# Optimization experiments

Measured on AMD Instinct MI355X. Metric: run time of the kernel, lower is better.

Reference implementation:

```python
import jax, jax.numpy as jnp
import numpy as np

KERNEL_SIZES = (3, 5, 7)
NUM_HEAD = 6
DIM = 192
K_SCALES = 3
HEADS_PER_SCALE = NUM_HEAD // K_SCALES  # 2
HEAD_DIM = DIM // NUM_HEAD              # 32
SCALE = HEAD_DIM ** -0.5


def _nbr_idx(L, K):
    # NATTEN non-causal, dilation=1: window centered on query, clamped at edges.
    start = jnp.clip(jnp.arange(L) - K // 2, 0, L - K)
    return start[:, None] + jnp.arange(K)  # [L, K]


def _na3d_branch(xi, K):
    # xi: [B, D, H, W, C] with C = 3 * HEADS_PER_SCALE * HEAD_DIM
    B, D, H, W, C = xi.shape
    qkv = xi.reshape(B, D, H, W, 3, HEADS_PER_SCALE, HEAD_DIM).transpose(4, 0, 5, 1, 2, 3, 6)
    q, k, v = qkv[0] * SCALE, qkv[1], qkv[2]  # each [B, h, D, H, W, hd]

    idd, idh, idw = _nbr_idx(D, K), _nbr_idx(H, K), _nbr_idx(W, K)

    def gather(t):
        t = jnp.take(t, idd, axis=2)  # [B,h,D,K,H,W,hd]
        t = jnp.take(t, idh, axis=4)  # [B,h,D,K,H,K,W,hd]
        t = jnp.take(t, idw, axis=6)  # [B,h,D,K,H,K,W,K,hd]
        return t

    kn = gather(k)
    vn = gather(v)
    # attention logits over the K^3 neighborhood per query
    attn = jnp.einsum('bndhwc,bndihjwkc->bndhwijk', q, kn)
    attn = jax.nn.softmax(attn.reshape(B, HEADS_PER_SCALE, D, H, W, K ** 3), axis=-1)
    attn = attn.reshape(B, HEADS_PER_SCALE, D, H, W, K, K, K)
    y = jnp.einsum('bndhwijk,bndihjwkc->bndhwc', attn, vn)
    # [B,h,D,H,W,hd] -> [B,D,H,W,h*hd]
    return y.transpose(0, 2, 3, 4, 1, 5).reshape(B, D, H, W, HEADS_PER_SCALE * HEAD_DIM)


def setup_inputs() -> dict:
    key = jax.random.key(0)
    k0, k1, k2 = jax.random.split(key, 3)
    x = jax.random.normal(k0, (1, 8, 24, 24, DIM), dtype=jnp.float32)
    W_qkv = jax.random.normal(k1, (DIM, 3 * DIM), dtype=jnp.float32) * 0.02
    b_qkv = jnp.zeros((3 * DIM,), dtype=jnp.float32)
    W_proj = jax.random.normal(k2, (DIM, DIM), dtype=jnp.float32) * 0.02
    b_proj = jnp.zeros((DIM,), dtype=jnp.float32)
    return {'x': x, 'W_qkv': W_qkv, 'b_qkv': b_qkv, 'W_proj': W_proj, 'b_proj': b_proj}


def reference(x, W_qkv, b_qkv, W_proj, b_proj):
    qkv = x @ W_qkv + b_qkv  # [B,D,H,W,3*DIM]
    # torch.split with channels [DIM, DIM, DIM]
    chunks = jnp.split(qkv, K_SCALES, axis=4)
    ys = [_na3d_branch(chunks[i], KERNEL_SIZES[i]) for i in range(K_SCALES)]
    y = jnp.concatenate(ys, axis=4)  # [B,D,H,W,DIM]
    return y @ W_proj + b_proj
```

## Files before the change

kernel.cpp:

```cpp
#include <hip/hip_runtime.h>

typedef unsigned short ushort_t;
typedef unsigned int uint_t;
typedef __attribute__((ext_vector_type(8))) short short8;
typedef __attribute__((ext_vector_type(4))) float f32x4;

constexpr int DD = 8, HH = 24, WW = 24;
constexpr int NQ = DD * HH * WW;
constexpr int CIN = 192;
constexpr int CQKV = 576;
constexpr int KP = 576;
constexpr float ATT_SCALE = 0.17677669529663687f;
constexpr int NROW = DD * HH;

__device__ __forceinline__ ushort_t bf16h(float x) {
    uint_t u = __float_as_uint(x);
    u += 0x7FFFu + ((u >> 16) & 1u);
    return (ushort_t)(u >> 16);
}
__device__ __forceinline__ float bf16f(ushort_t h) {
    return __uint_as_float(((uint_t)h) << 16);
}
__device__ __forceinline__ void unpack8(uint4 u, float* f) {
    f[0] = __uint_as_float(u.x << 16); f[1] = __uint_as_float(u.x & 0xffff0000u);
    f[2] = __uint_as_float(u.y << 16); f[3] = __uint_as_float(u.y & 0xffff0000u);
    f[4] = __uint_as_float(u.z << 16); f[5] = __uint_as_float(u.z & 0xffff0000u);
    f[6] = __uint_as_float(u.w << 16); f[7] = __uint_as_float(u.w & 0xffff0000u);
}

__global__ __launch_bounds__(256)
void convert_w_kernel(const float* __restrict__ Wq, const float* __restrict__ Wp,
                      ushort_t* __restrict__ Bq, ushort_t* __restrict__ Bp)
{
    __shared__ float T[32][36];
    int b = blockIdx.x;
    const float* W; ushort_t* Bb; int N;
    int kt, nt;
    if (b < 108) { W = Wq; Bb = Bq; N = CQKV; kt = b % 6; nt = b / 6; }
    else         { b -= 108; W = Wp; Bb = Bp; N = CIN; kt = b % 6; nt = b / 6; }
    const int k0 = kt * 32, n0 = nt * 32;
    const int tid = threadIdx.x;

    #pragma unroll
    for (int p = 0; p < 4; ++p) {
        int e = p * 256 + tid;
        int r = e >> 5, c = e & 31;
        T[c][r] = W[(long)(k0 + r) * N + n0 + c];
    }
    __syncthreads();
    const int n = tid >> 3;
    const int k4 = (tid & 7) * 4;
    float4 v = *(const float4*)(&T[n][k4]);
    ushort4 hv, lv;
    hv.x = bf16h(v.x); lv.x = bf16h(v.x - bf16f(hv.x));
    hv.y = bf16h(v.y); lv.y = bf16h(v.y - bf16f(hv.y));
    hv.z = bf16h(v.z); lv.z = bf16h(v.z - bf16f(hv.z));
    hv.w = bf16h(v.w); lv.w = bf16h(v.w - bf16f(hv.w));
    ushort_t* row = Bb + (long)(n0 + n) * KP + k0 + k4;
    *(ushort4*)(row)           = hv;
    *(ushort4*)(row + CIN)     = hv;
    *(ushort4*)(row + 2 * CIN) = lv;
}

template<bool BF16OUT>
__global__ __launch_bounds__(256)
void gemm_mfma_kernel(const float* __restrict__ A, const ushort_t* __restrict__ Bb,
                      const float* __restrict__ bias, void* __restrict__ Cout, int N)
{
    __shared__ ushort_t As[64][72];
    __shared__ ushort_t Bs[64][72];
    __shared__ float Ct[64][68];

    const int tid = threadIdx.x;
    const int bm = blockIdx.x * 64;
    const int bn = blockIdx.y * 64;

    const int wv = tid >> 6;
    const int lane = tid & 63;
    const int lm = lane & 15;
    const int quad = lane >> 4;
    const int wr = (wv >> 1) * 32;
    const int wc = (wv & 1) * 32;

    const int ar = tid >> 4;
    const int ac4 = (tid & 15) * 4;
    const int br0 = tid >> 3;
    const int bc0 = (tid & 7) * 8;

    f32x4 acc[2][2] = {};

    for (int kk = 0; kk < KP; kk += 64) {
        const int p3 = kk / 192;
        const int k0 = kk - p3 * 192;
        float4 av[4];
        #pragma unroll
        for (int p = 0; p < 4; ++p)
            av[p] = *(const float4*)(A + (long)(bm + ar + p * 16) * CIN + k0 + ac4);
        uint4 b0 = *(const uint4*)(Bb + (long)(bn + br0) * KP + kk + bc0);
        uint4 b1 = *(const uint4*)(Bb + (long)(bn + br0 + 32) * KP + kk + bc0);
        __syncthreads();
        #pragma unroll
        for (int p = 0; p < 4; ++p) {
            float4 v = av[p];
            ushort4 hv;
            hv.x = bf16h(v.x); hv.y = bf16h(v.y); hv.z = bf16h(v.z); hv.w = bf16h(v.w);
            if (p3 == 1) {
                hv.x = bf16h(v.x - bf16f(hv.x));
                hv.y = bf16h(v.y - bf16f(hv.y));
                hv.z = bf16h(v.z - bf16f(hv.z));
                hv.w = bf16h(v.w - bf16f(hv.w));
            }
            *(ushort4*)(&As[ar + p * 16][ac4]) = hv;
        }
        *(uint4*)(&Bs[br0][bc0]) = b0;
        *(uint4*)(&Bs[br0 + 32][bc0]) = b1;
        __syncthreads();

        #pragma unroll
        for (int ks = 0; ks < 64; ks += 32) {
            short8 af0 = *(const short8*)(&As[wr + lm][ks + quad * 8]);
            short8 af1 = *(const short8*)(&As[wr + 16 + lm][ks + quad * 8]);
            short8 bf0 = *(const short8*)(&Bs[wc + lm][ks + quad * 8]);
            short8 bf1 = *(const short8*)(&Bs[wc + 16 + lm][ks + quad * 8]);
            acc[0][0] = __builtin_amdgcn_mfma_f32_16x16x32_bf16(af0, bf0, acc[0][0], 0, 0, 0);
            acc[0][1] = __builtin_amdgcn_mfma_f32_16x16x32_bf16(af0, bf1, acc[0][1], 0, 0, 0);
            acc[1][0] = __builtin_amdgcn_mfma_f32_16x16x32_bf16(af1, bf0, acc[1][0], 0, 0, 0);
            acc[1][1] = __builtin_amdgcn_mfma_f32_16x16x32_bf16(af1, bf1, acc[1][1], 0, 0, 0);
        }
    }

    #pragma unroll
    for (int tc = 0; tc < 2; ++tc) {
        const float bv = bias[bn + wc + tc * 16 + lm];
        #pragma unroll
        for (int tr = 0; tr < 2; ++tr) {
            #pragma unroll
            for (int reg = 0; reg < 4; ++reg)
                Ct[wr + tr * 16 + quad * 4 + reg][wc + tc * 16 + lm] = acc[tr][tc][reg] + bv;
        }
    }
    __syncthreads();
    const int orow = tid >> 4;
    const int oc4 = (tid & 15) * 4;
    #pragma unroll
    for (int p = 0; p < 4; ++p) {
        const int r = orow + p * 16;
        float4 v = *(const float4*)(&Ct[r][oc4]);
        if (BF16OUT) {
            ushort4 hv;
            hv.x = bf16h(v.x); hv.y = bf16h(v.y); hv.z = bf16h(v.z); hv.w = bf16h(v.w);
            *(ushort4*)((ushort_t*)Cout + (long)(bm + r) * N + bn + oc4) = hv;
        } else {
            *(float4*)((float*)Cout + (long)(bm + r) * N + bn + oc4) = v;
        }
    }
}

constexpr int KROW = 72;
constexpr int RBUF = WW * KROW;

constexpr int EB0 = 0;
constexpr int EB1 = NROW * 2 * WW * 2;
constexpr int EB2 = EB1 + NROW * 3 * WW * 2;
constexpr int ETOT = EB2 + NROW * 4 * WW * 2;

template<int K>
__device__ __forceinline__
void split_chunk(const ushort_t* __restrict__ qkv,
                 float* __restrict__ accs, float* __restrict__ stats,
                 int r, int c, int nchunks, int scale, int ebase,
                 int w, int hd, int d8, int tid,
                 ushort_t* __restrict__ ksh, ushort_t* __restrict__ vsh)
{
    const int i0 = 2 * c;
    const int ni = (K - i0) < 2 ? (K - i0) : 2;
    const int NT = ni * K;

    const int dq = r / HH, hq = r % HH;
    int sd = dq - K / 2; sd = sd < 0 ? 0 : (sd > DD - K ? DD - K : sd);
    int sh = hq - K / 2; sh = sh < 0 ? 0 : (sh > HH - K ? HH - K : sh);
    int sw = w  - K / 2; sw = sw < 0 ? 0 : (sw > WW - K ? WW - K : sw);

    const int q = (dq * HH + hq) * WW + w;

    uint4 qu = *(const uint4*)(qkv + (long)q * CQKV + scale * 192 + hd * 32 + d8 * 8);
    float qf[8];
    unpack8(qu, qf);
    #pragma unroll
    for (int t = 0; t < 8; ++t) qf[t] *= ATT_SCALE;

    const int lw = tid >> 3;
    const int c8 = (tid & 7) * 8;

    auto load_kv = [&](int buf, int t) {
        int i = i0 + t / K;
        int j = t - (t / K) * K;
        const ushort_t* p = qkv + (long)(((sd + i) * HH + (sh + j)) * WW + lw) * CQKV
                          + scale * 192 + c8;
        uint4 kk = *(const uint4*)(p + 64);
        uint4 vv = *(const uint4*)(p + 128);
        *(uint4*)(ksh + buf * RBUF + lw * KROW + c8) = kk;
        *(uint4*)(vsh + buf * RBUF + lw * KROW + c8) = vv;
    };

    float m = -1e30f, sum = 0.f;
    float acc[8] = {};
    const int choff = hd * 32 + d8 * 8;

    load_kv(0, 0);
    if (NT > 1) load_kv(1, 1);

    for (int t = 0; t < NT; ++t) {
        __syncthreads();
        if (t + 2 < NT) load_kv((t + 2) % 3, t + 2);

        const ushort_t* kb = ksh + (t % 3) * RBUF + choff;
        float lg[K];
        #pragma unroll
        for (int n = 0; n < K; ++n) {
            uint4 ku = *(const uint4*)(kb + (sw + n) * KROW);
            float kf[8];
            unpack8(ku, kf);
            float p = qf[0] * kf[0] + qf[1] * kf[1] + qf[2] * kf[2] + qf[3] * kf[3]
                    + qf[4] * kf[4] + qf[5] * kf[5] + qf[6] * kf[6] + qf[7] * kf[7];
            p += __shfl_xor(p, 1);
            p += __shfl_xor(p, 2);
            lg[n] = p;
        }
        float mloc = lg[0];
        #pragma unroll
        for (int n = 1; n < K; ++n) mloc = fmaxf(mloc, lg[n]);
        float mnew = fmaxf(m, mloc);
        float alpha = __expf(m - mnew);
        m = mnew;
        sum *= alpha;
        #pragma unroll
        for (int d = 0; d < 8; ++d) acc[d] *= alpha;

        const ushort_t* vb = vsh + (t % 3) * RBUF + choff;
        #pragma unroll
        for (int n = 0; n < K; ++n) {
            float pr = __expf(lg[n] - mnew);
            sum += pr;
            uint4 vu = *(const uint4*)(vb + (sw + n) * KROW);
            float vf[8];
            unpack8(vu, vf);
            #pragma unroll
            for (int d = 0; d < 8; ++d) acc[d] += pr * vf[d];
        }
    }

    const int e = ebase + ((r * nchunks + c) * WW + w) * 2 + hd;
    if (d8 == 0) {
        stats[2 * e]     = m;
        stats[2 * e + 1] = sum;
    }
    float* ap = accs + (long)e * 32 + d8 * 8;
    *(float4*)(ap)     = make_float4(acc[0], acc[1], acc[2], acc[3]);
    *(float4*)(ap + 4) = make_float4(acc[4], acc[5], acc[6], acc[7]);
}

__global__ __launch_bounds__(192)
void na3d_split_kernel(const ushort_t* __restrict__ qkv,
                       float* __restrict__ accs, float* __restrict__ stats)
{
    __shared__ alignas(16) ushort_t ksh[3 * RBUF];
    __shared__ alignas(16) ushort_t vsh[3 * RBUF];

    const int tid = threadIdx.x;
    const int w  = tid >> 3;
    const int hd = (tid >> 2) & 1;
    const int d8 = tid & 3;

    const int bid = blockIdx.x;
    if (bid < NROW * 4) {
        int r = bid >> 2, c = bid & 3;
        split_chunk<7>(qkv, accs, stats, r, c, 4, 2, EB2, w, hd, d8, tid, ksh, vsh);
    } else if (bid < NROW * 4 + NROW * 3) {
        int t = bid - NROW * 4;
        int r = t / 3, c = t - (t / 3) * 3;
        split_chunk<5>(qkv, accs, stats, r, c, 3, 1, EB1, w, hd, d8, tid, ksh, vsh);
    } else {
        int t = bid - NROW * 7;
        int r = t >> 1, c = t & 1;
        split_chunk<3>(qkv, accs, stats, r, c, 2, 0, EB0, w, hd, d8, tid, ksh, vsh);
    }
}

__global__ __launch_bounds__(256)
void na3d_combine_kernel(const float* __restrict__ accs,
                         const float* __restrict__ stats,
                         float* __restrict__ y)
{
    const int n = blockIdx.x * 256 + threadIdx.x;
    constexpr int PER_SCALE = NROW * WW * 2 * 8;
    const int scale = n / PER_SCALE;
    const int rem = n - scale * PER_SCALE;
    const int d4 = rem & 7;
    const int hd = (rem >> 3) & 1;
    const int t  = rem >> 4;
    const int w  = t % WW;
    const int row = t / WW;

    const int CK = scale == 0 ? 2 : (scale == 1 ? 3 : 4);
    const int ebase = scale == 0 ? EB0 : (scale == 1 ? EB1 : EB2);

    float mv[4], sv[4];
    float M = -1e30f;
    for (int c = 0; c < CK; ++c) {
        int e = ebase + ((row * CK + c) * WW + w) * 2 + hd;
        mv[c] = stats[2 * e];
        sv[c] = stats[2 * e + 1];
        M = fmaxf(M, mv[c]);
    }
    float S = 0.f;
    float4 o = make_float4(0.f, 0.f, 0.f, 0.f);
    for (int c = 0; c < CK; ++c) {
        int e = ebase + ((row * CK + c) * WW + w) * 2 + hd;
        float wgt = __expf(mv[c] - M);
        S += sv[c] * wgt;
        float4 a = *(const float4*)(accs + (long)e * 32 + d4 * 4);
        o.x += wgt * a.x; o.y += wgt * a.y; o.z += wgt * a.z; o.w += wgt * a.w;
    }
    const float rs = 1.0f / S;
    o.x *= rs; o.y *= rs; o.z *= rs; o.w *= rs;

    const int q = row * WW + w;
    *(float4*)(y + (long)q * CIN + scale * 64 + hd * 32 + d4 * 4) = o;
}

extern "C" void kernel_launch(void* const* d_in, const int* in_sizes, int n_in,
                              void* d_out, int out_size, void* d_ws, size_t ws_size,
                              hipStream_t stream)
{
    const float* x      = (const float*)d_in[0];
    const float* W_qkv  = (const float*)d_in[1];
    const float* b_qkv  = (const float*)d_in[2];
    const float* W_proj = (const float*)d_in[3];
    const float* b_proj = (const float*)d_in[4];
    float* out = (float*)d_out;

    float* accs    = (float*)d_ws;
    float* stats   = accs + (long)ETOT * 32;
    float* y       = stats + 2 * ETOT;
    ushort_t* qkvb = (ushort_t*)(y + (long)NQ * CIN);
    ushort_t* Wbq  = qkvb + (long)NQ * CQKV;
    ushort_t* Wbp  = Wbq + (long)CQKV * KP;

    convert_w_kernel<<<dim3(144), 256, 0, stream>>>(W_qkv, W_proj, Wbq, Wbp);

    gemm_mfma_kernel<true><<<dim3(NQ / 64, CQKV / 64), 256, 0, stream>>>(x, Wbq, b_qkv, qkvb, CQKV);

    na3d_split_kernel<<<dim3(NROW * (4 + 3 + 2)), 192, 0, stream>>>(qkvb, accs, stats);
    na3d_combine_kernel<<<dim3(3 * NQ * 16 / 256), 256, 0, stream>>>(accs, stats, y);

    gemm_mfma_kernel<false><<<dim3(NQ / 64, CIN / 64), 256, 0, stream>>>(y, Wbp, b_proj, out, CIN);
}
```

Before: 122.7 us.

## Fuse split-softmax combine into output projection GEMM via shared-memory bf16 split

Merges the combine kernel (which merges partial softmax chunks into y) into the projection GEMM. Each block recomputes its 64 query rows of y across all 192 channels, splits them into bf16 hi/lo parts in shared memory, and runs MFMA against the converted W_proj. This drops one kernel launch and the fp32 y round trip through global memory. In exchange, each of the 3 column-blocks per row tile redoes the combine work, and the larger shared-memory footprint may lower occupancy.

```diff
diff --git a/kernel.cpp b/kernel.cpp
--- a/kernel.cpp
+++ b/kernel.cpp
@@ -27,6 +27,11 @@
     f[4] = __uint_as_float(u.z << 16); f[5] = __uint_as_float(u.z & 0xffff0000u);
     f[6] = __uint_as_float(u.w << 16); f[7] = __uint_as_float(u.w & 0xffff0000u);
 }
+
+constexpr int EB0 = 0;
+constexpr int EB1 = NROW * 2 * WW * 2;
+constexpr int EB2 = EB1 + NROW * 3 * WW * 2;
+constexpr int ETOT = EB2 + NROW * 4 * WW * 2;
 
 __global__ __launch_bounds__(256)
 void convert_w_kernel(const float* __restrict__ Wq, const float* __restrict__ Wp,
@@ -62,10 +67,9 @@
     *(ushort4*)(row + 2 * CIN) = lv;
 }
 
-template<bool BF16OUT>
 __global__ __launch_bounds__(256)
-void gemm_mfma_kernel(const float* __restrict__ A, const ushort_t* __restrict__ Bb,
-                      const float* __restrict__ bias, void* __restrict__ Cout, int N)
+void gemm1_kernel(const float* __restrict__ A, const ushort_t* __restrict__ Bb,
+                  const float* __restrict__ bias, ushort_t* __restrict__ Cout)
 {
     __shared__ ushort_t As[64][72];
     __shared__ ushort_t Bs[64][72];
@@ -74,6 +78,7 @@
     const int tid = threadIdx.x;
     const int bm = blockIdx.x * 64;
     const int bn = blockIdx.y * 64;
+    const int N = CQKV;
 
     const int wv = tid >> 6;
     const int lane = tid & 63;
@@ -146,23 +151,14 @@
     for (int p = 0; p < 4; ++p) {
         const int r = orow + p * 16;
         float4 v = *(const float4*)(&Ct[r][oc4]);
-        if (BF16OUT) {
-            ushort4 hv;
-            hv.x = bf16h(v.x); hv.y = bf16h(v.y); hv.z = bf16h(v.z); hv.w = bf16h(v.w);
-            *(ushort4*)((ushort_t*)Cout + (long)(bm + r) * N + bn + oc4) = hv;
-        } else {
-            *(float4*)((float*)Cout + (long)(bm + r) * N + bn + oc4) = v;
-        }
+        ushort4 hv;
+        hv.x = bf16h(v.x); hv.y = bf16h(v.y); hv.z = bf16h(v.z); hv.w = bf16h(v.w);
+        *(ushort4*)(Cout + (long)(bm + r) * N + bn + oc4) = hv;
     }
 }
 
 constexpr int KROW = 72;
 constexpr int RBUF = WW * KROW;
-
-constexpr int EB0 = 0;
-constexpr int EB1 = NROW * 2 * WW * 2;
-constexpr int EB2 = EB1 + NROW * 3 * WW * 2;
-constexpr int ETOT = EB2 + NROW * 4 * WW * 2;
 
 template<int K>
 __device__ __forceinline__
@@ -287,46 +283,125 @@
     }
 }
 
+constexpr int YST = 200;
+
 __global__ __launch_bounds__(256)
-void na3d_combine_kernel(const float* __restrict__ accs,
-                         const float* __restrict__ stats,
-                         float* __restrict__ y)
-{
-    const int n = blockIdx.x * 256 + threadIdx.x;
-    constexpr int PER_SCALE = NROW * WW * 2 * 8;
-    const int scale = n / PER_SCALE;
-    const int rem = n - scale * PER_SCALE;
-    const int d4 = rem & 7;
-    const int hd = (rem >> 3) & 1;
-    const int t  = rem >> 4;
-    const int w  = t % WW;
-    const int row = t / WW;
-
-    const int CK = scale == 0 ? 2 : (scale == 1 ? 3 : 4);
-    const int ebase = scale == 0 ? EB0 : (scale == 1 ? EB1 : EB2);
-
-    float mv[4], sv[4];
-    float M = -1e30f;
-    for (int c = 0; c < CK; ++c) {
-        int e = ebase + ((row * CK + c) * WW + w) * 2 + hd;
-        mv[c] = stats[2 * e];
-        sv[c] = stats[2 * e + 1];
-        M = fmaxf(M, mv[c]);
-    }
-    float S = 0.f;
-    float4 o = make_float4(0.f, 0.f, 0.f, 0.f);
-    for (int c = 0; c < CK; ++c) {
-        int e = ebase + ((row * CK + c) * WW + w) * 2 + hd;
-        float wgt = __expf(mv[c] - M);
-        S += sv[c] * wgt;
-        float4 a = *(const float4*)(accs + (long)e * 32 + d4 * 4);
-        o.x += wgt * a.x; o.y += wgt * a.y; o.z += wgt * a.z; o.w += wgt * a.w;
-    }
-    const float rs = 1.0f / S;
-    o.x *= rs; o.y *= rs; o.z *= rs; o.w *= rs;
-
-    const int q = row * WW + w;
-    *(float4*)(y + (long)q * CIN + scale * 64 + hd * 32 + d4 * 4) = o;
+void combine_gemm2_kernel(const float* __restrict__ accs, const float* __restrict__ stats,
+                          const ushort_t* __restrict__ Bb, const float* __restrict__ bias,
+                          float* __restrict__ out)
+{
+    __shared__ union {
+        struct { ushort_t yhi[64][YST]; ushort_t ylo[64][YST]; ushort_t Bs[64][72]; } s;
+        float Ct[64][68];
+    } u;
+
+    const int tid = threadIdx.x;
+    const int bm = blockIdx.x * 64;
+    const int bn = blockIdx.y * 64;
+
+    {
+        const int ql = tid >> 2;
+        const int q = bm + ql;
+        const int row = q / WW;
+        const int w = q - row * WW;
+        const int chb = (tid & 3) * 48;
+        #pragma unroll
+        for (int c4 = 0; c4 < 12; ++c4) {
+            const int ch = chb + c4 * 4;
+            const int scale = ch >> 6;
+            const int rem = ch & 63;
+            const int hd = rem >> 5;
+            const int d4 = (rem >> 2) & 7;
+            const int CK = scale == 0 ? 2 : (scale == 1 ? 3 : 4);
+            const int ebase = scale == 0 ? EB0 : (scale == 1 ? EB1 : EB2);
+
+            float mv[4], sv[4];
+            float M = -1e30f;
+            for (int c = 0; c < CK; ++c) {
+                int e = ebase + ((row * CK + c) * WW + w) * 2 + hd;
+                mv[c] = stats[2 * e];
+                sv[c] = stats[2 * e + 1];
+                M = fmaxf(M, mv[c]);
+            }
+            float S = 0.f;
+            float4 o = make_float4(0.f, 0.f, 0.f, 0.f);
+            for (int c = 0; c < CK; ++c) {
+                int e = ebase + ((row * CK + c) * WW + w) * 2 + hd;
+                float wgt = __expf(mv[c] - M);
+                S += sv[c] * wgt;
+                float4 a = *(const float4*)(accs + (long)e * 32 + d4 * 4);
+                o.x += wgt * a.x; o.y += wgt * a.y; o.z += wgt * a.z; o.w += wgt * a.w;
+            }
+            const float rs = 1.0f / S;
+            o.x *= rs; o.y *= rs; o.z *= rs; o.w *= rs;
+
+            ushort4 hv, lv;
+            hv.x = bf16h(o.x); lv.x = bf16h(o.x - bf16f(hv.x));
+            hv.y = bf16h(o.y); lv.y = bf16h(o.y - bf16f(hv.y));
+            hv.z = bf16h(o.z); lv.z = bf16h(o.z - bf16f(hv.z));
+            hv.w = bf16h(o.w); lv.w = bf16h(o.w - bf16f(hv.w));
+            *(ushort4*)(&u.s.yhi[ql][ch]) = hv;
+            *(ushort4*)(&u.s.ylo[ql][ch]) = lv;
+        }
+    }
+    __syncthreads();
+
+    const int wv = tid >> 6;
+    const int lane = tid & 63;
+    const int lm = lane & 15;
+    const int quad = lane >> 4;
+    const int wr = (wv >> 1) * 32;
+    const int wc = (wv & 1) * 32;
+
+    const int br0 = tid >> 3;
+    const int bc0 = (tid & 7) * 8;
+
+    f32x4 acc[2][2] = {};
+
+    for (int kk = 0; kk < KP; kk += 64) {
+        const int p3 = kk / 192;
+        const int k0 = kk - p3 * 192;
+        uint4 b0 = *(const uint4*)(Bb + (long)(bn + br0) * KP + kk + bc0);
+        uint4 b1 = *(const uint4*)(Bb + (long)(bn + br0 + 32) * KP + kk + bc0);
+        __syncthreads();
+        *(uint4*)(&u.s.Bs[br0][bc0]) = b0;
+        *(uint4*)(&u.s.Bs[br0 + 32][bc0]) = b1;
+        __syncthreads();
+
+        const ushort_t* ybase = (p3 == 1) ? &u.s.ylo[0][0] : &u.s.yhi[0][0];
+        #pragma unroll
+        for (int ks = 0; ks < 64; ks += 32) {
+            short8 af0 = *(const short8*)(ybase + (wr + lm) * YST + k0 + ks + quad * 8);
+            short8 af1 = *(const short8*)(ybase + (wr + 16 + lm) * YST + k0 + ks + quad * 8);
+            short8 bf0 = *(const short8*)(&u.s.Bs[wc + lm][ks + quad * 8]);
+            short8 bf1 = *(const short8*)(&u.s.Bs[wc + 16 + lm][ks + quad * 8]);
+            acc[0][0] = __builtin_amdgcn_mfma_f32_16x16x32_bf16(af0, bf0, acc[0][0], 0, 0, 0);
+            acc[0][1] = __builtin_amdgcn_mfma_f32_16x16x32_bf16(af0, bf1, acc[0][1], 0, 0, 0);
+            acc[1][0] = __builtin_amdgcn_mfma_f32_16x16x32_bf16(af1, bf0, acc[1][0], 0, 0, 0);
+            acc[1][1] = __builtin_amdgcn_mfma_f32_16x16x32_bf16(af1, bf1, acc[1][1], 0, 0, 0);
+        }
+    }
+
+    __syncthreads();
+    #pragma unroll
+    for (int tc = 0; tc < 2; ++tc) {
+        const float bv = bias[bn + wc + tc * 16 + lm];
+        #pragma unroll
+        for (int tr = 0; tr < 2; ++tr) {
+            #pragma unroll
+            for (int reg = 0; reg < 4; ++reg)
+                u.Ct[wr + tr * 16 + quad * 4 + reg][wc + tc * 16 + lm] = acc[tr][tc][reg] + bv;
+        }
+    }
+    __syncthreads();
+    const int orow = tid >> 4;
+    const int oc4 = (tid & 15) * 4;
+    #pragma unroll
+    for (int p = 0; p < 4; ++p) {
+        const int r = orow + p * 16;
+        float4 v = *(const float4*)(&u.Ct[r][oc4]);
+        *(float4*)(out + (long)(bm + r) * CIN + bn + oc4) = v;
+    }
 }
 
 extern "C" void kernel_launch(void* const* d_in, const int* in_sizes, int n_in,
@@ -342,17 +417,15 @@
 
     float* accs    = (float*)d_ws;
     float* stats   = accs + (long)ETOT * 32;
-    float* y       = stats + 2 * ETOT;
-    ushort_t* qkvb = (ushort_t*)(y + (long)NQ * CIN);
+    ushort_t* qkvb = (ushort_t*)(stats + 2 * ETOT);
     ushort_t* Wbq  = qkvb + (long)NQ * CQKV;
     ushort_t* Wbp  = Wbq + (long)CQKV * KP;
 
     convert_w_kernel<<<dim3(144), 256, 0, stream>>>(W_qkv, W_proj, Wbq, Wbp);
 
-    gemm_mfma_kernel<true><<<dim3(NQ / 64, CQKV / 64), 256, 0, stream>>>(x, Wbq, b_qkv, qkvb, CQKV);
+    gemm1_kernel<<<dim3(NQ / 64, CQKV / 64), 256, 0, stream>>>(x, Wbq, b_qkv, qkvb);
 
     na3d_split_kernel<<<dim3(NROW * (4 + 3 + 2)), 192, 0, stream>>>(qkvb, accs, stats);
-    na3d_combine_kernel<<<dim3(3 * NQ * 16 / 256), 256, 0, stream>>>(accs, stats, y);
-
-    gemm_mfma_kernel<false><<<dim3(NQ / 64, CIN / 64), 256, 0, stream>>>(y, Wbp, b_proj, out, CIN);
-}
+
+    combine_gemm2_kernel<<<dim3(NQ / 64, CIN / 64), 256, 0, stream>>>(accs, stats, Wbp, b_proj, out);
+}
```

New measurement: 133.2 us. +8.6%, slower.

## Fuse split-softmax combine into split kernel via last-block atomic counter

Applied to the files above, without the earlier changes.

Removes the separate combine kernel launch. Each split block atomically increments a per-row, per-scale counter, and the last block to finish a row merges all the chunk partials (max, sum, accumulators) and writes y. The counters are zeroed by the weight-conversion kernel. This saves one launch and its tail, at the cost of thread fences, an atomic per block, and serialized combine work in the last block of each row.

```diff
diff --git a/kernel.cpp b/kernel.cpp
--- a/kernel.cpp
+++ b/kernel.cpp
@@ -28,18 +28,27 @@
     f[6] = __uint_as_float(u.w << 16); f[7] = __uint_as_float(u.w & 0xffff0000u);
 }
 
+constexpr int EB0 = 0;
+constexpr int EB1 = NROW * 2 * WW * 2;
+constexpr int EB2 = EB1 + NROW * 3 * WW * 2;
+constexpr int ETOT = EB2 + NROW * 4 * WW * 2;
+
 __global__ __launch_bounds__(256)
 void convert_w_kernel(const float* __restrict__ Wq, const float* __restrict__ Wp,
-                      ushort_t* __restrict__ Bq, ushort_t* __restrict__ Bp)
+                      ushort_t* __restrict__ Bq, ushort_t* __restrict__ Bp,
+                      int* __restrict__ cnt)
 {
     __shared__ float T[32][36];
     int b = blockIdx.x;
+    const int tid = threadIdx.x;
+    if (b == 0) {
+        for (int i = tid; i < 3 * NROW; i += 256) cnt[i] = 0;
+    }
     const float* W; ushort_t* Bb; int N;
     int kt, nt;
     if (b < 108) { W = Wq; Bb = Bq; N = CQKV; kt = b % 6; nt = b / 6; }
     else         { b -= 108; W = Wp; Bb = Bp; N = CIN; kt = b % 6; nt = b / 6; }
     const int k0 = kt * 32, n0 = nt * 32;
-    const int tid = threadIdx.x;
 
     #pragma unroll
     for (int p = 0; p < 4; ++p) {
@@ -159,11 +168,6 @@
 constexpr int KROW = 72;
 constexpr int RBUF = WW * KROW;
 
-constexpr int EB0 = 0;
-constexpr int EB1 = NROW * 2 * WW * 2;
-constexpr int EB2 = EB1 + NROW * 3 * WW * 2;
-constexpr int ETOT = EB2 + NROW * 4 * WW * 2;
-
 template<int K>
 __device__ __forceinline__
 void split_chunk(const ushort_t* __restrict__ qkv,
@@ -262,71 +266,73 @@
 
 __global__ __launch_bounds__(192)
 void na3d_split_kernel(const ushort_t* __restrict__ qkv,
-                       float* __restrict__ accs, float* __restrict__ stats)
+                       float* __restrict__ accs, float* __restrict__ stats,
+                       float* __restrict__ y, int* __restrict__ cnt)
 {
     __shared__ alignas(16) ushort_t ksh[3 * RBUF];
     __shared__ alignas(16) ushort_t vsh[3 * RBUF];
+    __shared__ int lastflag;
 
     const int tid = threadIdx.x;
     const int w  = tid >> 3;
     const int hd = (tid >> 2) & 1;
     const int d8 = tid & 3;
 
+    int scale, r, c, nchunks, ebase;
     const int bid = blockIdx.x;
     if (bid < NROW * 4) {
-        int r = bid >> 2, c = bid & 3;
+        r = bid >> 2; c = bid & 3; scale = 2; nchunks = 4; ebase = EB2;
         split_chunk<7>(qkv, accs, stats, r, c, 4, 2, EB2, w, hd, d8, tid, ksh, vsh);
-    } else if (bid < NROW * 4 + NROW * 3) {
+    } else if (bid < NROW * 7) {
         int t = bid - NROW * 4;
-        int r = t / 3, c = t - (t / 3) * 3;
+        r = t / 3; c = t - (t / 3) * 3; scale = 1; nchunks = 3; ebase = EB1;
         split_chunk<5>(qkv, accs, stats, r, c, 3, 1, EB1, w, hd, d8, tid, ksh, vsh);
     } else {
         int t = bid - NROW * 7;
-        int r = t >> 1, c = t & 1;
+        r = t >> 1; c = t & 1; scale = 0; nchunks = 2; ebase = EB0;
         split_chunk<3>(qkv, accs, stats, r, c, 2, 0, EB0, w, hd, d8, tid, ksh, vsh);
     }
-}
-
-__global__ __launch_bounds__(256)
-void na3d_combine_kernel(const float* __restrict__ accs,
-                         const float* __restrict__ stats,
-                         float* __restrict__ y)
-{
-    const int n = blockIdx.x * 256 + threadIdx.x;
-    constexpr int PER_SCALE = NROW * WW * 2 * 8;
-    const int scale = n / PER_SCALE;
-    const int rem = n - scale * PER_SCALE;
-    const int d4 = rem & 7;
-    const int hd = (rem >> 3) & 1;
-    const int t  = rem >> 4;
-    const int w  = t % WW;
-    const int row = t / WW;
-
-    const int CK = scale == 0 ? 2 : (scale == 1 ? 3 : 4);
-    const int ebase = scale == 0 ? EB0 : (scale == 1 ? EB1 : EB2);
-
-    float mv[4], sv[4];
-    float M = -1e30f;
-    for (int c = 0; c < CK; ++c) {
-        int e = ebase + ((row * CK + c) * WW + w) * 2 + hd;
-        mv[c] = stats[2 * e];
-        sv[c] = stats[2 * e + 1];
-        M = fmaxf(M, mv[c]);
-    }
-    float S = 0.f;
-    float4 o = make_float4(0.f, 0.f, 0.f, 0.f);
-    for (int c = 0; c < CK; ++c) {
-        int e = ebase + ((row * CK + c) * WW + w) * 2 + hd;
-        float wgt = __expf(mv[c] - M);
-        S += sv[c] * wgt;
-        float4 a = *(const float4*)(accs + (long)e * 32 + d4 * 4);
-        o.x += wgt * a.x; o.y += wgt * a.y; o.z += wgt * a.z; o.w += wgt * a.w;
-    }
-    const float rs = 1.0f / S;
-    o.x *= rs; o.y *= rs; o.z *= rs; o.w *= rs;
-
-    const int q = row * WW + w;
-    *(float4*)(y + (long)q * CIN + scale * 64 + hd * 32 + d4 * 4) = o;
+
+    __threadfence();
+    if (tid == 0) {
+        int old = atomicAdd(&cnt[scale * NROW + r], 1);
+        lastflag = (old == nchunks - 1);
+    }
+    __syncthreads();
+    if (!lastflag) return;
+    __threadfence();
+
+    const int CK = nchunks;
+    #pragma unroll
+    for (int pass = 0; pass < 2; ++pass) {
+        const int e2 = pass * 192 + tid;
+        const int cd4 = e2 & 7;
+        const int chd = (e2 >> 3) & 1;
+        const int cw  = e2 >> 4;
+
+        float mv[4], sv[4];
+        float M = -1e30f;
+        for (int cc = 0; cc < CK; ++cc) {
+            int e = ebase + ((r * CK + cc) * WW + cw) * 2 + chd;
+            mv[cc] = stats[2 * e];
+            sv[cc] = stats[2 * e + 1];
+            M = fmaxf(M, mv[cc]);
+        }
+        float S = 0.f;
+        float4 o = make_float4(0.f, 0.f, 0.f, 0.f);
+        for (int cc = 0; cc < CK; ++cc) {
+            int e = ebase + ((r * CK + cc) * WW + cw) * 2 + chd;
+            float wgt = __expf(mv[cc] - M);
+            S += sv[cc] * wgt;
+            float4 a = *(const float4*)(accs + (long)e * 32 + cd4 * 4);
+            o.x += wgt * a.x; o.y += wgt * a.y; o.z += wgt * a.z; o.w += wgt * a.w;
+        }
+        const float rs = 1.0f / S;
+        o.x *= rs; o.y *= rs; o.z *= rs; o.w *= rs;
+
+        const int q = r * WW + cw;
+        *(float4*)(y + (long)q * CIN + scale * 64 + chd * 32 + cd4 * 4) = o;
+    }
 }
 
 extern "C" void kernel_launch(void* const* d_in, const int* in_sizes, int n_in,
@@ -346,13 +352,13 @@
     ushort_t* qkvb = (ushort_t*)(y + (long)NQ * CIN);
     ushort_t* Wbq  = qkvb + (long)NQ * CQKV;
     ushort_t* Wbp  = Wbq + (long)CQKV * KP;
-
-    convert_w_kernel<<<dim3(144), 256, 0, stream>>>(W_qkv, W_proj, Wbq, Wbp);
+    int* cnt       = (int*)(Wbp + (long)CIN * KP);
+
+    convert_w_kernel<<<dim3(144), 256, 0, stream>>>(W_qkv, W_proj, Wbq, Wbp, cnt);
 
     gemm_mfma_kernel<true><<<dim3(NQ / 64, CQKV / 64), 256, 0, stream>>>(x, Wbq, b_qkv, qkvb, CQKV);
 
-    na3d_split_kernel<<<dim3(NROW * (4 + 3 + 2)), 192, 0, stream>>>(qkvb, accs, stats);
-    na3d_combine_kernel<<<dim3(3 * NQ * 16 / 256), 256, 0, stream>>>(accs, stats, y);
+    na3d_split_kernel<<<dim3(NROW * (4 + 3 + 2)), 192, 0, stream>>>(qkvb, accs, stats, y, cnt);
 
     gemm_mfma_kernel<false><<<dim3(NQ / 64, CIN / 64), 256, 0, stream>>>(y, Wbp, b_proj, out, CIN);
 }
```

Result: slower. 326.6 us (+166.2%).
